# Kernel tuning notes

Measured on AMD Instinct MI355X. Metric: run time of the kernel, lower is better.

Reference implementation:

```python
import jax, jax.numpy as jnp
import numpy as np

EMBED = 256
HEADS = 8
HD = EMBED // HEADS
LEVELS = 4
POINTS = 4
FFN_H = 1024
BS = 8
LQ = 900
SHAPES = [(100, 100), (50, 50), (25, 25), (13, 13)]


def setup_inputs() -> dict:
    key = jax.random.key(0)
    ks = jax.random.split(key, 20)
    nv = sum(h * w for h, w in SHAPES)
    starts = np.cumsum([0] + [h * w for h, w in SHAPES])[:-1]
    inp = {
        "queries": jax.random.normal(ks[0], (BS, LQ, EMBED), jnp.float32),
        "memory": jax.random.normal(ks[1], (BS, nv, EMBED), jnp.float32),
        "query_pos": jax.random.normal(ks[2], (BS, LQ, EMBED), jnp.float32),
        "reference_points": jax.random.uniform(ks[3], (BS, LQ, LEVELS, 4), jnp.float32) * 0.9 + 0.05,
        "spatial_shapes": jnp.asarray(SHAPES, jnp.int32),
        "level_start_index": jnp.asarray(starts, jnp.int32),
    }
    def lin(k, din, dout):
        k1, k2 = jax.random.split(k)
        w = jax.random.normal(k1, (din, dout), jnp.float32) * 0.02
        b = jax.random.normal(k2, (dout,), jnp.float32) * 0.01
        return w, b
    specs = [("Wq", "bq", EMBED, EMBED), ("Wk", "bk", EMBED, EMBED), ("Wv", "bv", EMBED, EMBED),
             ("Wo", "bo", EMBED, EMBED), ("Wvd", "bvd", EMBED, EMBED),
             ("Woff", "boff", EMBED, HEADS * LEVELS * POINTS * 2),
             ("Watt", "batt", EMBED, HEADS * LEVELS * POINTS),
             ("Wop", "bop", EMBED, EMBED), ("Wg", "bg", 2 * EMBED, 2 * EMBED),
             ("W1", "b1", EMBED, FFN_H), ("W2", "b2", FFN_H, EMBED)]
    for i, (wn, bn, di, do) in enumerate(specs):
        w, b = lin(ks[4 + i], di, do)
        inp[wn] = w
        inp[bn] = b
    for n in ["ln1", "ln2", "ln3"]:
        inp[n + "_s"] = jnp.ones((EMBED,), jnp.float32)
        inp[n + "_b"] = jnp.zeros((EMBED,), jnp.float32)
    return inp


def _ln(x, s, b):
    m = jnp.mean(x, -1, keepdims=True)
    v = jnp.mean(jnp.square(x - m), -1, keepdims=True)
    return (x - m) * jax.lax.rsqrt(v + 1e-5) * s + b


def _bilinear(v_l, lx, ly, H, W):
    # v_l: [bs,h,H*W,hd]; lx,ly: [bs,h,lq,p] normalized in [0,1]
    # grid_sample(align_corners=False, padding=zeros) semantics
    px = lx * W - 0.5
    py = ly * H - 0.5
    x0 = jnp.floor(px)
    y0 = jnp.floor(py)
    wx = px - x0
    wy = py - y0
    x0i = x0.astype(jnp.int32)
    y0i = y0.astype(jnp.int32)
    bs, h, lq, p = lx.shape
    out = jnp.zeros((bs, h, lq, p, HD), v_l.dtype)
    for dy in (0, 1):
        for dx in (0, 1):
            xi = x0i + dx
            yi = y0i + dy
            w = (wx if dx else 1.0 - wx) * (wy if dy else 1.0 - wy)
            valid = (xi >= 0) & (xi < W) & (yi >= 0) & (yi < H)
            idx = jnp.clip(yi, 0, H - 1) * W + jnp.clip(xi, 0, W - 1)
            g = jnp.take_along_axis(v_l, idx.reshape(bs, h, lq * p)[..., None], axis=2)
            g = g.reshape(bs, h, lq, p, HD)
            out = out + w[..., None] * jnp.where(valid[..., None], g, 0.0)
    return out


def reference(queries, memory, query_pos, reference_points, spatial_shapes, level_start_index,
              Wq, bq, Wk, bk, Wv, bv, Wo, bo, Wvd, bvd, Woff, boff, Watt, batt, Wop, bop,
              Wg, bg, W1, b1, W2, b2, ln1_s, ln1_b, ln2_s, ln2_b, ln3_s, ln3_b):
    bs, lq, _ = queries.shape
    shp = np.asarray(spatial_shapes)
    st = np.asarray(level_start_index)

    # ---- self attention (pre-norm, q=k=x+pos, v=x) ----
    x = _ln(queries, ln1_s, ln1_b)
    qk = x + query_pos
    Q = (qk @ Wq + bq).reshape(bs, lq, HEADS, HD)
    K = (qk @ Wk + bk).reshape(bs, lq, HEADS, HD)
    V = (x @ Wv + bv).reshape(bs, lq, HEADS, HD)
    scores = jnp.einsum('bqhd,bkhd->bhqk', Q, K) * (1.0 / np.sqrt(HD))
    attn = jax.nn.softmax(scores, axis=-1)
    sa = jnp.einsum('bhqk,bkhd->bqhd', attn, V).reshape(bs, lq, EMBED) @ Wo + bo
    x1 = queries + sa  # dropout is identity in eval

    # ---- MS-deformable cross attention ----
    y = _ln(x1, ln2_s, ln2_b)
    qc = y + query_pos
    val = (memory @ Wvd + bvd).reshape(bs, -1, HEADS, HD).transpose(0, 2, 1, 3)  # [bs,h,Nv,hd]
    off = (qc @ Woff + boff).reshape(bs, lq, HEADS, LEVELS, POINTS, 2)
    aw = jax.nn.softmax((qc @ Watt + batt).reshape(bs, lq, HEADS, LEVELS * POINTS), axis=-1)
    aw = aw.reshape(bs, lq, HEADS, LEVELS, POINTS)
    rp = reference_points[:, :, None, :, None, :]  # [bs,lq,1,L,1,4]
    loc = rp[..., :2] + off / POINTS * rp[..., 2:] * 0.5  # [bs,lq,h,L,p,2]

    out = jnp.zeros((bs, HEADS, lq, HD), queries.dtype)
    for l in range(LEVELS):
        H, W = int(shp[l, 0]), int(shp[l, 1])
        s0 = int(st[l])
        v_l = val[:, :, s0:s0 + H * W]
        lx = jnp.transpose(loc[:, :, :, l, :, 0], (0, 2, 1, 3))  # [bs,h,lq,p]
        ly = jnp.transpose(loc[:, :, :, l, :, 1], (0, 2, 1, 3))
        samp = _bilinear(v_l, lx, ly, H, W)  # [bs,h,lq,p,hd]
        w = jnp.transpose(aw[:, :, :, l], (0, 2, 1, 3))  # [bs,h,lq,p]
        out = out + jnp.sum(w[..., None] * samp, axis=3)
    cross = out.transpose(0, 2, 1, 3).reshape(bs, lq, EMBED) @ Wop + bop

    # ---- gated fusion ----
    gi = jnp.concatenate([x1, cross], axis=-1)
    g = jax.nn.sigmoid(gi @ Wg + bg)
    x2 = g[..., :EMBED] * x1 + g[..., EMBED:] * cross

    # ---- FFN ----
    z = _ln(x2, ln3_s, ln3_b)
    ffn = jax.nn.relu(z @ W1 + b1) @ W2 + b2
    return (x2 + ffn, aw, loc)
```

## Files before the change

kernel.cpp:

```cpp
#include <hip/hip_runtime.h>
#include <hip/hip_bf16.h>
#include <math.h>

#define BB 8
#define LQ 900
#define EE 256
#define NH 8
#define HD 32
#define NL 4
#define NP 4
#define FFN_H 1024

typedef __bf16 bf16x8 __attribute__((ext_vector_type(8)));
typedef float f32x4 __attribute__((ext_vector_type(4)));
typedef unsigned short u16x8 __attribute__((ext_vector_type(8)));

__device__ __forceinline__ unsigned short f2b(float f) {
    union { float f; unsigned int u; } v; v.f = f;
    unsigned int u = v.u;
    unsigned int r = (u + 0x7fffu + ((u >> 16) & 1u)) >> 16;
    return (unsigned short)r;
}
__device__ __forceinline__ float b2f(unsigned short h) {
    union { unsigned int u; float f; } v; v.u = ((unsigned int)h) << 16; return v.f;
}

typedef __attribute__((address_space(3))) unsigned int* lds_ptr_t;
typedef const __attribute__((address_space(1))) unsigned int* gbl_ptr_t;
#define GLOAD16(g, l) __builtin_amdgcn_global_load_lds((gbl_ptr_t)(g), (lds_ptr_t)(l), 16, 0, 0)
#define VMCNT(n) asm volatile("s_waitcnt vmcnt(" #n ")" ::: "memory")

struct TDesc { const float* src; unsigned short* dst; int K, N, tile0; };
struct TPack {
    TDesc d[11];
    const float *bq, *bk, *boff, *batt;
    float *bqk, *boa;
};

__global__ __launch_bounds__(256) void prep_kernel(
    TPack p,
    const float* __restrict__ queries, const float* __restrict__ qpos,
    const float* __restrict__ ln1_s, const float* __restrict__ ln1_b,
    unsigned short* __restrict__ x_b, unsigned short* __restrict__ qk_b,
    const float* __restrict__ mem, unsigned short* __restrict__ mem_b, long memN)
{
    const int bi = blockIdx.x;
    const int t = threadIdx.x;

    if (bi < 1248) {
        int di = 0;
#pragma unroll
        for (int i = 1; i < 11; ++i) if (bi >= p.d[i].tile0) di = i;
        TDesc d = p.d[di];
        int tt = bi - d.tile0;
        int tn = (d.N + 31) >> 5;
        int tk = tt / tn, tc = tt % tn;
        __shared__ float tile[32][33];
        int tx = t & 31, ty = t >> 5;
#pragma unroll
        for (int i = 0; i < 4; ++i) {
            int kk = tk * 32 + ty + i * 8, nn = tc * 32 + tx;
            tile[ty + i * 8][tx] = d.src[(size_t)kk * d.N + nn];
        }
        __syncthreads();
#pragma unroll
        for (int i = 0; i < 4; ++i) {
            int nn = tc * 32 + ty + i * 8, kk = tk * 32 + tx;
            d.dst[(size_t)nn * d.K + kk] = f2b(tile[tx][ty + i * 8]);
        }
        return;
    }
    if (bi < 1252) {
        int which = bi - 1248;
        if (which == 0)      p.bqk[t] = p.bq[t];
        else if (which == 1) p.bqk[256 + t] = p.bk[t];
        else if (which == 2) p.boa[t] = p.boff[t];
        else if (t < 128)    p.boa[256 + t] = p.batt[t];
        return;
    }
    if (bi < 1252 + BB * LQ) {
        const int row = bi - 1252;
        const int w = t >> 6, lane = t & 63;
        __shared__ float red[4];
        float v = queries[(size_t)row * EE + t];
        float sum = v;
#pragma unroll
        for (int o = 32; o; o >>= 1) sum += __shfl_xor(sum, o, 64);
        if (lane == 0) red[w] = sum;
        __syncthreads();
        float mean = (red[0] + red[1] + red[2] + red[3]) * (1.0f / 256.0f);
        __syncthreads();
        float dd = v - mean;
        float sq = dd * dd;
#pragma unroll
        for (int o = 32; o; o >>= 1) sq += __shfl_xor(sq, o, 64);
        if (lane == 0) red[w] = sq;
        __syncthreads();
        float var = (red[0] + red[1] + red[2] + red[3]) * (1.0f / 256.0f);
        float y = dd * rsqrtf(var + 1e-5f) * ln1_s[t] + ln1_b[t];
        x_b[(size_t)row * EE + t]  = f2b(y);
        qk_b[(size_t)row * EE + t] = f2b(y + qpos[(size_t)row * EE + t]);
        return;
    }
    {
        long i = ((long)(bi - 1252 - BB * LQ) * 256 + t) * 8;
        long stride = (long)2048 * 256 * 8;
        for (; i < memN; i += stride) {
            float4 a = *(const float4*)(mem + i);
            float4 b = *(const float4*)(mem + i + 4);
            u16x8 o;
            o[0] = f2b(a.x); o[1] = f2b(a.y); o[2] = f2b(a.z); o[3] = f2b(a.w);
            o[4] = f2b(b.x); o[5] = f2b(b.y); o[6] = f2b(b.z); o[7] = f2b(b.w);
            *(u16x8*)(mem_b + i) = o;
        }
    }
}

struct GD {
    const unsigned short* A;
    const unsigned short* Bt;
    const float* bias;
    const float* resid;
    float* outF;
    unsigned short* outB;
    const float* lnS; const float* lnB; const float* lnAdd;
    unsigned short* lnOut;
    int M, K, N, ntN, tile0, ldOutB, outBoff, act;
};
struct GB { GD d[3]; int nd, tot; };

template<int BN>
__global__ __launch_bounds__(256, (BN == 128) ? 4 : 2) void gemm_pipe(GB g) {
    __shared__ __align__(16) unsigned short ldsb[2][(64 + BN) * 32];
    __shared__ float lnred[2][64][2];
    const int tid = threadIdx.x;
    const int l = tid & 63, w = tid >> 6;
    const int wr = w >> 1, wc = w & 1;
    constexpr int NJ = BN / 32;

    int t = blockIdx.x;
    if (t >= g.tot) return;
    int d = 0;
    while (d + 1 < g.nd && t >= g.d[d + 1].tile0) ++d;

    auto stage = [&](int dd, int tt, int ks, int pp) {
        const GD& D = g.d[dd];
        int local = tt - D.tile0;
        int m0 = (local / D.ntN) * 64;
        int n0 = (local % D.ntN) * BN;
        unsigned short* base = &ldsb[pp][0];
        {
            int row = w * 16 + (l >> 2);
            int rg = m0 + row; int mm = D.M - 1; rg = rg < mm ? rg : mm;
            int schunk = ((l & 3) ^ ((row >> 1) & 3)) << 4;
            GLOAD16((const char*)(D.A + (size_t)rg * D.K + (ks << 5)) + schunk,
                    base + (w * 16) * 32);
        }
#pragma unroll
        for (int ib = 0; ib < BN / 64; ++ib) {
            int row = ib * 64 + w * 16 + (l >> 2);
            int rg = n0 + row; int nn = D.N - 1; rg = rg < nn ? rg : nn;
            int schunk = ((l & 3) ^ ((row >> 1) & 3)) << 4;
            GLOAD16((const char*)(D.Bt + (size_t)rg * D.K + (ks << 5)) + schunk,
                    base + 2048 + (ib * 64 + w * 16) * 32);
        }
    };

    stage(d, t, 0, 0);
    int p = 0;

    while (true) {
        const GD D = g.d[d];
        int local = t - D.tile0;
        const int m0 = (local / D.ntN) * 64;
        const int n0 = (local % D.ntN) * BN;
        const int nk = D.K >> 5;

        f32x4 acc[2][NJ];
#pragma unroll
        for (int i = 0; i < 2; ++i)
#pragma unroll
            for (int j = 0; j < NJ; ++j) acc[i][j] = (f32x4){0.f, 0.f, 0.f, 0.f};

        for (int ks = 0; ks < nk; ++ks) {
            int nt = t, nks = ks + 1, ndd = d;
            bool have = true;
            if (nks == nk) {
                nt = t + gridDim.x; nks = 0;
                if (nt >= g.tot) have = false;
                else { while (ndd + 1 < g.nd && nt >= g.d[ndd + 1].tile0) ++ndd; }
            }
            if (have) {
                stage(ndd, nt, nks, p ^ 1);
                if constexpr (BN == 128) { VMCNT(3); } else { VMCNT(5); }
            } else {
                VMCNT(0);
            }
            __builtin_amdgcn_sched_barrier(0);
            __builtin_amdgcn_s_barrier();
            __builtin_amdgcn_sched_barrier(0);
            {
                const char* base = (const char*)&ldsb[p][0];
                const int rch = ((l >> 4) ^ ((l >> 1) & 3)) << 4;
                bf16x8 af[2];
#pragma unroll
                for (int i = 0; i < 2; ++i) {
                    int row = wr * 32 + i * 16 + (l & 15);
                    af[i] = *(const bf16x8*)(base + row * 64 + rch);
                }
#pragma unroll
                for (int j = 0; j < NJ; ++j) {
                    int row = wc * (BN / 2) + j * 16 + (l & 15);
                    bf16x8 bfr = *(const bf16x8*)(base + 4096 + row * 64 + rch);
#pragma unroll
                    for (int i = 0; i < 2; ++i)
                        acc[i][j] = __builtin_amdgcn_mfma_f32_16x16x32_bf16(af[i], bfr, acc[i][j], 0, 0, 0);
                }
            }
            __builtin_amdgcn_sched_barrier(0);
            __builtin_amdgcn_s_barrier();
            __builtin_amdgcn_sched_barrier(0);
            p ^= 1;
        }

#pragma unroll
        for (int i = 0; i < 2; ++i) {
#pragma unroll
            for (int r = 0; r < 4; ++r) {
                int gm = m0 + wr * 32 + i * 16 + ((l >> 4) << 2) + r;
                if (gm >= D.M) continue;
#pragma unroll
                for (int j = 0; j < NJ; ++j) {
                    int gn = n0 + wc * (BN / 2) + j * 16 + (l & 15);
                    if (gn >= D.N) continue;
                    float v = acc[i][j][r];
                    if (D.bias)  v += D.bias[gn];
                    if (D.resid) v += D.resid[(size_t)gm * D.N + gn];
                    if (D.act == 1)      v = fmaxf(v, 0.f);
                    else if (D.act == 2) v = 1.0f / (1.0f + __expf(-v));
                    acc[i][j][r] = v;
                    if (D.outF) D.outF[(size_t)gm * D.N + gn] = v;
                    if (D.outB) D.outB[(size_t)gm * D.ldOutB + D.outBoff + gn] = f2b(v);
                }
            }
        }

        if constexpr (BN == 256) {
            if (D.lnOut) {
#pragma unroll
                for (int i = 0; i < 2; ++i) {
#pragma unroll
                    for (int r = 0; r < 4; ++r) {
                        float s1 = 0.f, s2 = 0.f;
#pragma unroll
                        for (int j = 0; j < NJ; ++j) {
                            float v = acc[i][j][r];
                            s1 += v; s2 += v * v;
                        }
#pragma unroll
                        for (int o = 1; o <= 8; o <<= 1) {
                            s1 += __shfl_xor(s1, o, 64);
                            s2 += __shfl_xor(s2, o, 64);
                        }
                        if ((l & 15) == 0) {
                            int row = wr * 32 + i * 16 + ((l >> 4) << 2) + r;
                            lnred[wc][row][0] = s1;
                            lnred[wc][row][1] = s2;
                        }
                    }
                }
                __syncthreads();
#pragma unroll
                for (int i = 0; i < 2; ++i) {
#pragma unroll
                    for (int r = 0; r < 4; ++r) {
                        int row = wr * 32 + i * 16 + ((l >> 4) << 2) + r;
                        int gm = m0 + row;
                        if (gm >= D.M) continue;
                        float mean = (lnred[0][row][0] + lnred[1][row][0]) * (1.0f / 256.0f);
                        float msq  = (lnred[0][row][1] + lnred[1][row][1]) * (1.0f / 256.0f);
                        float rs = rsqrtf(msq - mean * mean + 1e-5f);
#pragma unroll
                        for (int j = 0; j < NJ; ++j) {
                            int gn = wc * (BN / 2) + j * 16 + (l & 15);
                            float y = (acc[i][j][r] - mean) * rs * D.lnS[gn] + D.lnB[gn]
                                      + D.lnAdd[(size_t)gm * 256 + gn];
                            D.lnOut[(size_t)gm * 256 + gn] = f2b(y);
                        }
                    }
                }
            }
        }

        t += gridDim.x;
        if (t >= g.tot) break;
        while (d + 1 < g.nd && t >= g.d[d + 1].tile0) ++d;
    }
}

__global__ __launch_bounds__(256) void attn_mfma(
    const unsigned short* __restrict__ QK, const unsigned short* __restrict__ Vb,
    unsigned short* __restrict__ outB)
{
    const int qt = blockIdx.x;
    const int bh = blockIdx.y;
    const int b = bh >> 3, h = bh & 7;
    const int tid = threadIdx.x;
    const int w = tid >> 6, l = tid & 63;

    __shared__ __align__(16) unsigned short Ks[64 * 32];
    __shared__ __align__(16) unsigned short VT[32 * 64];
    __shared__ __align__(16) unsigned short Ps[4][64 * 20];

    const int qrow_w = qt * 64 + w * 16;
    int qr = qrow_w + (l & 15); qr = qr < LQ ? qr : LQ - 1;
    bf16x8 qf = *(const bf16x8*)(QK + ((size_t)(b * LQ + qr)) * 512 + h * 32 + (l >> 4) * 8);

    f32x4 acc0 = {0.f, 0.f, 0.f, 0.f}, acc1 = {0.f, 0.f, 0.f, 0.f};
    float m_run = -1e30f, l_run = 0.f;
    const float scale = 0.17677669529663689f;
    const f32x4 z4 = {0.f, 0.f, 0.f, 0.f};

    const int key = tid >> 2;
    const int dg = (tid & 3) * 8;
    u16x8 kvc, vvc, kvn, vvn;
    {
        int krow = key; krow = krow < LQ ? krow : LQ - 1;
        size_t base = (size_t)(b * LQ + krow);
        kvc = *(const u16x8*)(QK + base * 512 + 256 + h * 32 + dg);
        vvc = *(const u16x8*)(Vb + base * 256 + h * 32 + dg);
    }

    for (int kt = 0; kt < 15; ++kt) {
        __syncthreads();
        *(u16x8*)((char*)Ks + key * 64 + ((dg * 2) ^ ((key & 3) << 4))) = kvc;
#pragma unroll
        for (int e = 0; e < 8; ++e) {
            int dd = dg + e;
            *(unsigned short*)((char*)VT + dd * 128 + ((key * 2) ^ ((dd & 7) << 4))) = vvc[e];
        }
        if (kt < 14) {
            int krow = (kt + 1) * 64 + key; krow = krow < LQ ? krow : LQ - 1;
            size_t base = (size_t)(b * LQ + krow);
            kvn = *(const u16x8*)(QK + base * 512 + 256 + h * 32 + dg);
            vvn = *(const u16x8*)(Vb + base * 256 + h * 32 + dg);
        }
        __syncthreads();

        float p[4][4];
        float tmax = -1e30f;
#pragma unroll
        for (int m = 0; m < 4; ++m) {
            int kr = m * 16 + (l & 15);
            bf16x8 kf = *(const bf16x8*)((const char*)Ks + kr * 64 +
                        (((l >> 4) * 16) ^ ((kr & 3) << 4)));
            f32x4 sf = __builtin_amdgcn_mfma_f32_16x16x32_bf16(kf, qf, z4, 0, 0, 0);
#pragma unroll
            for (int r = 0; r < 4; ++r) {
                int kk = kt * 64 + m * 16 + (l >> 4) * 4 + r;
                float sv = (kk < LQ) ? sf[r] * scale : -1e30f;
                p[m][r] = sv;
                tmax = fmaxf(tmax, sv);
            }
        }
        tmax = fmaxf(tmax, __shfl_xor(tmax, 16, 64));
        tmax = fmaxf(tmax, __shfl_xor(tmax, 32, 64));
        float newm = fmaxf(m_run, tmax);
        float corr = __expf(m_run - newm);
        m_run = newm;
        float tsum = 0.f;
#pragma unroll
        for (int m = 0; m < 4; ++m)
#pragma unroll
            for (int r = 0; r < 4; ++r) {
                float e = __expf(p[m][r] - newm);
                p[m][r] = e;
                tsum += e;
            }
        tsum += __shfl_xor(tsum, 16, 64);
        tsum += __shfl_xor(tsum, 32, 64);
        l_run = l_run * corr + tsum;
        acc0 *= corr;
        acc1 *= corr;

        unsigned short* pw = &Ps[w][0];
#pragma unroll
        for (int m = 0; m < 4; ++m)
#pragma unroll
            for (int r = 0; r < 4; ++r) {
                int kk = m * 16 + (l >> 4) * 4 + r;
                pw[kk * 20 + (l & 15)] = f2b(p[m][r]);
            }

#pragma unroll
        for (int s = 0; s < 2; ++s) {
            union { unsigned short u[8]; bf16x8 v; } pb;
#pragma unroll
            for (int j = 0; j < 8; ++j)
                pb.u[j] = pw[(s * 32 + (l >> 4) * 8 + j) * 20 + (l & 15)];
#pragma unroll
            for (int m2 = 0; m2 < 2; ++m2) {
                int dd = m2 * 16 + (l & 15);
                bf16x8 vf = *(const bf16x8*)((const char*)VT + dd * 128 +
                            ((s * 64 + (l >> 4) * 16) ^ ((dd & 7) << 4)));
                if (m2 == 0) acc0 = __builtin_amdgcn_mfma_f32_16x16x32_bf16(vf, pb.v, acc0, 0, 0, 0);
                else         acc1 = __builtin_amdgcn_mfma_f32_16x16x32_bf16(vf, pb.v, acc1, 0, 0, 0);
            }
        }
        if (kt < 14) { kvc = kvn; vvc = vvn; }
    }

    float inv = 1.0f / l_run;
    int q = qrow_w + (l & 15);
    if (q < LQ) {
        size_t obase = ((size_t)(b * LQ + q)) * 256 + h * 32;
#pragma unroll
        for (int r = 0; r < 4; ++r) {
            int d0 = (l >> 4) * 4 + r;
            outB[obase + d0]      = f2b(acc0[r] * inv);
            outB[obase + 16 + d0] = f2b(acc1[r] * inv);
        }
    }
}

__global__ __launch_bounds__(256) void sample_fused(
    const float* __restrict__ off_att, const float* __restrict__ refp,
    const unsigned short* __restrict__ val,
    const int* __restrict__ shapes, const int* __restrict__ starts,
    float* __restrict__ aw_out, float* __restrict__ loc_out,
    unsigned short* __restrict__ samp, int NV)
{
    const int row = blockIdx.x;
    const int b = row / LQ;
    const int t = threadIdx.x;
    const int h = t >> 5, d = t & 31;

    __shared__ float l_logit[128];
    __shared__ float l_aw[128];
    __shared__ float l_loc[256];
    __shared__ int l_sh[NL * 2];
    __shared__ int l_st[NL];

    if (t < 128) l_logit[t] = off_att[(size_t)row * 384 + 256 + t];
    {
        float o = off_att[(size_t)row * 384 + t];
        int c = t & 1;
        int lv = (t >> 3) & 3;
        float rc = refp[((size_t)row * 4 + lv) * 4 + c];
        float rs = refp[((size_t)row * 4 + lv) * 4 + 2 + c];
        float loc = rc + o * 0.125f * rs;
        l_loc[t] = loc;
        loc_out[(size_t)row * 256 + t] = loc;
    }
    if (t < NL * 2) l_sh[t] = shapes[t];
    if (t < NL) l_st[t] = starts[t];
    __syncthreads();
    if (t < 128) {
        int hh = t >> 4;
        float mx = -1e30f;
#pragma unroll
        for (int i = 0; i < 16; ++i) mx = fmaxf(mx, l_logit[hh * 16 + i]);
        float sum = 0.f;
#pragma unroll
        for (int i = 0; i < 16; ++i) sum += __expf(l_logit[hh * 16 + i] - mx);
        float aw = __expf(l_logit[t] - mx) / sum;
        l_aw[t] = aw;
        aw_out[(size_t)row * 128 + t] = aw;
    }
    __syncthreads();

    float acc = 0.f;
    const unsigned short* vb = val + (size_t)b * NV * EE + h * HD + d;

#pragma unroll
    for (int lv = 0; lv < NL; ++lv) {
        const int Hh = l_sh[lv * 2], Ww = l_sh[lv * 2 + 1];
        const int s0 = l_st[lv];
#pragma unroll
        for (int p = 0; p < NP; ++p) {
            const int base = ((h * NL + lv) * NP + p) * 2;
            float lx = l_loc[base], ly = l_loc[base + 1];
            float wgt0 = l_aw[h * 16 + lv * NP + p];
            float px = lx * (float)Ww - 0.5f;
            float py = ly * (float)Hh - 0.5f;
            float x0f = floorf(px), y0f = floorf(py);
            float wx = px - x0f, wy = py - y0f;
            int x0 = (int)x0f, y0 = (int)y0f;
#pragma unroll
            for (int dy = 0; dy < 2; ++dy) {
                int yi = y0 + dy;
                bool vy = (yi >= 0) && (yi < Hh);
                int yc = min(max(yi, 0), Hh - 1);
                float wyv = dy ? wy : 1.f - wy;
#pragma unroll
                for (int dx = 0; dx < 2; ++dx) {
                    int xi = x0 + dx;
                    bool vv = vy && (xi >= 0) && (xi < Ww);
                    int xc = min(max(xi, 0), Ww - 1);
                    float wgt = wgt0 * wyv * (dx ? wx : 1.f - wx);
                    float gv = b2f(vb[(size_t)(s0 + yc * Ww + xc) * EE]);
                    acc += vv ? wgt * gv : 0.f;
                }
            }
        }
    }
    samp[(size_t)row * EE + t] = f2b(acc);
}

__global__ __launch_bounds__(256) void gate_ln3(
    const float* __restrict__ g, const float* __restrict__ x1,
    const float* __restrict__ cross, const float* __restrict__ s,
    const float* __restrict__ bln, float* __restrict__ x2out,
    unsigned short* __restrict__ zb)
{
    const int row = blockIdx.x;
    const int t = threadIdx.x;
    const int w = t >> 6;
    const int lane = t & 63;
    __shared__ float red[4];

    float g1 = g[(size_t)row * 512 + t];
    float g2 = g[(size_t)row * 512 + 256 + t];
    float v = g1 * x1[(size_t)row * EE + t] + g2 * cross[(size_t)row * EE + t];
    x2out[(size_t)row * EE + t] = v;

    float sum = v;
#pragma unroll
    for (int o = 32; o; o >>= 1) sum += __shfl_xor(sum, o, 64);
    if (lane == 0) red[w] = sum;
    __syncthreads();
    float mean = (red[0] + red[1] + red[2] + red[3]) * (1.0f / 256.0f);
    __syncthreads();

    float d = v - mean;
    float sq = d * d;
#pragma unroll
    for (int o = 32; o; o >>= 1) sq += __shfl_xor(sq, o, 64);
    if (lane == 0) red[w] = sq;
    __syncthreads();
    float var = (red[0] + red[1] + red[2] + red[3]) * (1.0f / 256.0f);

    float y = d * rsqrtf(var + 1e-5f) * s[t] + bln[t];
    zb[(size_t)row * EE + t] = f2b(y);
}

extern "C" void kernel_launch(void* const* d_in, const int* in_sizes, int n_in,
                              void* d_out, int out_size, void* d_ws, size_t ws_size,
                              hipStream_t stream)
{
    const float* queries   = (const float*)d_in[0];
    const float* memory    = (const float*)d_in[1];
    const float* query_pos = (const float*)d_in[2];
    const float* refp      = (const float*)d_in[3];
    const int*   shapes    = (const int*)d_in[4];
    const int*   starts    = (const int*)d_in[5];
    const float* Wq  = (const float*)d_in[6],  *bq  = (const float*)d_in[7];
    const float* Wk  = (const float*)d_in[8],  *bk  = (const float*)d_in[9];
    const float* Wv  = (const float*)d_in[10], *bv  = (const float*)d_in[11];
    const float* Wo  = (const float*)d_in[12], *bo  = (const float*)d_in[13];
    const float* Wvd = (const float*)d_in[14], *bvd = (const float*)d_in[15];
    const float* Woff= (const float*)d_in[16], *boff= (const float*)d_in[17];
    const float* Watt= (const float*)d_in[18], *batt= (const float*)d_in[19];
    const float* Wop = (const float*)d_in[20], *bop = (const float*)d_in[21];
    const float* Wg  = (const float*)d_in[22], *bg  = (const float*)d_in[23];
    const float* W1  = (const float*)d_in[24], *b1  = (const float*)d_in[25];
    const float* W2  = (const float*)d_in[26], *b2  = (const float*)d_in[27];
    const float* ln1_s = (const float*)d_in[28], *ln1_b = (const float*)d_in[29];
    const float* ln2_s = (const float*)d_in[30], *ln2_b = (const float*)d_in[31];
    const float* ln3_s = (const float*)d_in[32], *ln3_b = (const float*)d_in[33];

    const int NV = in_sizes[1] / (BB * EE);
    const int Mq = BB * LQ;
    const int Mv = BB * NV;
    const long memN = (long)Mv * EE;

    char* W8 = (char*)d_ws;
    size_t off = 0;
    auto alloc = [&](size_t bytes) { char* p = W8 + off; off += (bytes + 255) & ~(size_t)255; return p; };

    unsigned short* mem_b = (unsigned short*)alloc((size_t)memN * 2);
    unsigned short* val_b = (unsigned short*)alloc((size_t)memN * 2);
    unsigned short* WtQK  = (unsigned short*)alloc(512 * 256 * 2);
    unsigned short* WtV   = (unsigned short*)alloc(256 * 256 * 2);
    unsigned short* WtO   = (unsigned short*)alloc(256 * 256 * 2);
    unsigned short* WtVD  = (unsigned short*)alloc(256 * 256 * 2);
    unsigned short* WtOA  = (unsigned short*)alloc(384 * 256 * 2);
    unsigned short* WtOP  = (unsigned short*)alloc(256 * 256 * 2);
    unsigned short* WtG   = (unsigned short*)alloc(512 * 512 * 2);
    unsigned short* Wt1   = (unsigned short*)alloc(1024 * 256 * 2);
    unsigned short* Wt2   = (unsigned short*)alloc(256 * 1024 * 2);
    float*          bqk   = (float*)alloc(512 * 4);
    float*          boa   = (float*)alloc(384 * 4);
    unsigned short* qkb   = (unsigned short*)alloc((size_t)Mq * 512 * 2);
    unsigned short* vb_buf= (unsigned short*)alloc((size_t)Mq * 256 * 2);
    unsigned short* av_buf= (unsigned short*)alloc((size_t)Mq * 256 * 2);
    float*          x1    = (float*)alloc((size_t)Mq * 256 * 4);
    unsigned short* xc_cat= (unsigned short*)alloc((size_t)Mq * 512 * 2);
    unsigned short* qc_b  = (unsigned short*)alloc((size_t)Mq * 256 * 2);
    unsigned short* qk_b  = (unsigned short*)alloc((size_t)Mq * 256 * 2);
    float*          cross = (float*)alloc((size_t)Mq * 256 * 4);

    unsigned short* x_b = (unsigned short*)cross;
    float* off_att = (float*)qkb;
    unsigned short* samp_b = av_buf;
    float* gbuf = (float*)mem_b;
    float* x2   = (float*)((char*)mem_b + (size_t)Mq * 512 * 4);
    unsigned short* z_b = (unsigned short*)((char*)x2 + (size_t)Mq * 256 * 4);
    unsigned short* hidden_b = (unsigned short*)((char*)z_b + (size_t)Mq * 256 * 2);

    float* out0    = (float*)d_out;
    float* aw_out  = out0 + (size_t)Mq * 256;
    float* loc_out = aw_out + (size_t)Mq * 128;

    dim3 blk(256);
    const int tMq = (Mq + 63) / 64;
    const int tv  = (Mv + 63) / 64;

    TPack tp;
    tp.d[0]  = { Wq,   WtQK,             256, 256,    0 };
    tp.d[1]  = { Wk,   WtQK + 256 * 256, 256, 256,   64 };
    tp.d[2]  = { Wv,   WtV,              256, 256,  128 };
    tp.d[3]  = { Wo,   WtO,              256, 256,  192 };
    tp.d[4]  = { Wvd,  WtVD,             256, 256,  256 };
    tp.d[5]  = { Woff, WtOA,             256, 256,  320 };
    tp.d[6]  = { Watt, WtOA + 256 * 256, 256, 128,  384 };
    tp.d[7]  = { Wop,  WtOP,             256, 256,  416 };
    tp.d[8]  = { Wg,   WtG,              512, 512,  480 };
    tp.d[9]  = { W1,   Wt1,              256, 1024, 736 };
    tp.d[10] = { W2,   Wt2,             1024, 256,  992 };
    tp.bq = bq; tp.bk = bk; tp.boff = boff; tp.batt = batt;
    tp.bqk = bqk; tp.boa = boa;
    prep_kernel<<<1252 + Mq + 2048, blk, 0, stream>>>(
        tp, queries, query_pos, ln1_s, ln1_b, x_b, qk_b, memory, mem_b, memN);

    {
        GB g; g.nd = 3;
        g.d[0] = { mem_b, WtVD, bvd, nullptr, nullptr, val_b,
                   nullptr, nullptr, nullptr, nullptr,
                   Mv, 256, 256, 2, 0, 256, 0, 0 };
        g.d[1] = { qk_b, WtQK, bqk, nullptr, nullptr, qkb,
                   nullptr, nullptr, nullptr, nullptr,
                   Mq, 256, 512, 4, tv * 2, 512, 0, 0 };
        g.d[2] = { x_b, WtV, bv, nullptr, nullptr, vb_buf,
                   nullptr, nullptr, nullptr, nullptr,
                   Mq, 256, 256, 2, tv * 2 + tMq * 4, 256, 0, 0 };
        g.tot = tv * 2 + tMq * 6;
        gemm_pipe<128><<<1536, blk, 0, stream>>>(g);
    }

    attn_mfma<<<dim3(15, BB * NH), blk, 0, stream>>>(qkb, vb_buf, av_buf);

    {
        GB g; g.nd = 1;
        g.d[0] = { av_buf, WtO, bo, queries, x1, xc_cat,
                   ln2_s, ln2_b, query_pos, qc_b,
                   Mq, 256, 256, 1, 0, 512, 0, 0 };
        g.tot = tMq;
        gemm_pipe<256><<<tMq, blk, 0, stream>>>(g);
    }

    {
        GB g; g.nd = 1;
        g.d[0] = { qc_b, WtOA, boa, nullptr, off_att, nullptr,
                   nullptr, nullptr, nullptr, nullptr,
                   Mq, 256, 384, 3, 0, 384, 0, 0 };
        g.tot = tMq * 3;
        gemm_pipe<128><<<tMq * 3, blk, 0, stream>>>(g);
    }

    sample_fused<<<Mq, blk, 0, stream>>>(off_att, refp, val_b, shapes, starts,
                                         aw_out, loc_out, samp_b, NV);

    {
        GB g; g.nd = 1;
        g.d[0] = { samp_b, WtOP, bop, nullptr, cross, xc_cat,
                   nullptr, nullptr, nullptr, nullptr,
                   Mq, 256, 256, 2, 0, 512, 256, 0 };
        g.tot = tMq * 2;
        gemm_pipe<128><<<tMq * 2, blk, 0, stream>>>(g);
    }

    {
        GB g; g.nd = 1;
        g.d[0] = { xc_cat, WtG, bg, nullptr, gbuf, nullptr,
                   nullptr, nullptr, nullptr, nullptr,
                   Mq, 512, 512, 4, 0, 512, 0, 2 };
        g.tot = tMq * 4;
        gemm_pipe<128><<<tMq * 4, blk, 0, stream>>>(g);
    }

    gate_ln3<<<Mq, blk, 0, stream>>>(gbuf, x1, cross, ln3_s, ln3_b, x2, z_b);

    {
        GB g; g.nd = 1;
        g.d[0] = { z_b, Wt1, b1, nullptr, nullptr, hidden_b,
                   nullptr, nullptr, nullptr, nullptr,
                   Mq, 256, 1024, 8, 0, 1024, 0, 1 };
        g.tot = tMq * 8;
        gemm_pipe<128><<<tMq * 8, blk, 0, stream>>>(g);
    }

    {
        GB g; g.nd = 1;
        g.d[0] = { hidden_b, Wt2, b2, x2, out0, nullptr,
                   nullptr, nullptr, nullptr, nullptr,
                   Mq, 1024, 256, 2, 0, 256, 0, 0 };
        g.tot = tMq * 2;
        gemm_pipe<128><<<tMq * 2, blk, 0, stream>>>(g);
    }
}
```

Measured before the change: 333.6 us.

## Fuse fp32-to-bf16 memory conversion into value-projection GEMM A-tile loads

Removes the separate pass in the prep kernel that converted the whole fp32 memory tensor to bf16. The value GEMM now reads fp32 rows directly into registers, converts them and writes the swizzled bf16 A tile into LDS after the MFMA step. The value projection is split into its own launch with BN=256, apart from the QK/V projections. This saves a full write and re-read of a bf16 copy of memory, at the cost of more register pressure, extra LDS stores and lgkm waits inside the GEMM loop, and an extra kernel launch.

```diff
diff --git a/kernel.cpp b/kernel.cpp
--- a/kernel.cpp
+++ b/kernel.cpp
@@ -29,6 +29,7 @@
 typedef const __attribute__((address_space(1))) unsigned int* gbl_ptr_t;
 #define GLOAD16(g, l) __builtin_amdgcn_global_load_lds((gbl_ptr_t)(g), (lds_ptr_t)(l), 16, 0, 0)
 #define VMCNT(n) asm volatile("s_waitcnt vmcnt(" #n ")" ::: "memory")
+#define LGKM0()  asm volatile("s_waitcnt lgkmcnt(0)" ::: "memory")
 
 struct TDesc { const float* src; unsigned short* dst; int K, N, tile0; };
 struct TPack {
@@ -41,8 +42,7 @@
     TPack p,
     const float* __restrict__ queries, const float* __restrict__ qpos,
     const float* __restrict__ ln1_s, const float* __restrict__ ln1_b,
-    unsigned short* __restrict__ x_b, unsigned short* __restrict__ qk_b,
-    const float* __restrict__ mem, unsigned short* __restrict__ mem_b, long memN)
+    unsigned short* __restrict__ x_b, unsigned short* __restrict__ qk_b)
 {
     const int bi = blockIdx.x;
     const int t = threadIdx.x;
@@ -78,7 +78,7 @@
         else if (t < 128)    p.boa[256 + t] = p.batt[t];
         return;
     }
-    if (bi < 1252 + BB * LQ) {
+    {
         const int row = bi - 1252;
         const int w = t >> 6, lane = t & 63;
         __shared__ float red[4];
@@ -100,24 +100,12 @@
         float y = dd * rsqrtf(var + 1e-5f) * ln1_s[t] + ln1_b[t];
         x_b[(size_t)row * EE + t]  = f2b(y);
         qk_b[(size_t)row * EE + t] = f2b(y + qpos[(size_t)row * EE + t]);
-        return;
-    }
-    {
-        long i = ((long)(bi - 1252 - BB * LQ) * 256 + t) * 8;
-        long stride = (long)2048 * 256 * 8;
-        for (; i < memN; i += stride) {
-            float4 a = *(const float4*)(mem + i);
-            float4 b = *(const float4*)(mem + i + 4);
-            u16x8 o;
-            o[0] = f2b(a.x); o[1] = f2b(a.y); o[2] = f2b(a.z); o[3] = f2b(a.w);
-            o[4] = f2b(b.x); o[5] = f2b(b.y); o[6] = f2b(b.z); o[7] = f2b(b.w);
-            *(u16x8*)(mem_b + i) = o;
-        }
     }
 }
 
 struct GD {
     const unsigned short* A;
+    const float* Af;
     const unsigned short* Bt;
     const float* bias;
     const float* resid;
@@ -129,7 +117,7 @@
 };
 struct GB { GD d[3]; int nd, tot; };
 
-template<int BN>
+template<int BN, bool AF32>
 __global__ __launch_bounds__(256, (BN == 128) ? 4 : 2) void gemm_pipe(GB g) {
     __shared__ __align__(16) unsigned short ldsb[2][(64 + BN) * 32];
     __shared__ float lnred[2][64][2];
@@ -143,13 +131,23 @@
     int d = 0;
     while (d + 1 < g.nd && t >= g.d[d + 1].tile0) ++d;
 
+    const int sc = tid & 3;
+    float4 fA[2];
+
     auto stage = [&](int dd, int tt, int ks, int pp) {
         const GD& D = g.d[dd];
         int local = tt - D.tile0;
         int m0 = (local / D.ntN) * 64;
         int n0 = (local % D.ntN) * BN;
         unsigned short* base = &ldsb[pp][0];
-        {
+        if constexpr (AF32) {
+            int row = tid >> 2;
+            int rg = m0 + row; int mm = D.M - 1; rg = rg < mm ? rg : mm;
+            int ck = (sc ^ ((row >> 1) & 3)) * 8;
+            const float* src = D.Af + (size_t)rg * D.K + (ks << 5) + ck;
+            fA[0] = *(const float4*)src;
+            fA[1] = *(const float4*)(src + 4);
+        } else {
             int row = w * 16 + (l >> 2);
             int rg = m0 + row; int mm = D.M - 1; rg = rg < mm ? rg : mm;
             int schunk = ((l & 3) ^ ((row >> 1) & 3)) << 4;
@@ -165,8 +163,16 @@
                     base + 2048 + (ib * 64 + w * 16) * 32);
         }
     };
+    auto commitA = [&](int pp) {
+        int row = tid >> 2;
+        u16x8 o;
+        o[0] = f2b(fA[0].x); o[1] = f2b(fA[0].y); o[2] = f2b(fA[0].z); o[3] = f2b(fA[0].w);
+        o[4] = f2b(fA[1].x); o[5] = f2b(fA[1].y); o[6] = f2b(fA[1].z); o[7] = f2b(fA[1].w);
+        *(u16x8*)((char*)&ldsb[pp][0] + row * 64 + sc * 16) = o;
+    };
 
     stage(d, t, 0, 0);
+    if constexpr (AF32) { commitA(0); LGKM0(); }
     int p = 0;
 
     while (true) {
@@ -192,7 +198,9 @@
             }
             if (have) {
                 stage(ndd, nt, nks, p ^ 1);
-                if constexpr (BN == 128) { VMCNT(3); } else { VMCNT(5); }
+                if constexpr (AF32)          { VMCNT(6); }
+                else if constexpr (BN == 128){ VMCNT(3); }
+                else                         { VMCNT(5); }
             } else {
                 VMCNT(0);
             }
@@ -216,6 +224,9 @@
                     for (int i = 0; i < 2; ++i)
                         acc[i][j] = __builtin_amdgcn_mfma_f32_16x16x32_bf16(af[i], bfr, acc[i][j], 0, 0, 0);
                 }
+            }
+            if constexpr (AF32) {
+                if (have) { commitA(p ^ 1); LGKM0(); }
             }
             __builtin_amdgcn_sched_barrier(0);
             __builtin_amdgcn_s_barrier();
@@ -245,7 +256,7 @@
             }
         }
 
-        if constexpr (BN == 256) {
+        if constexpr (BN == 256 && !AF32) {
             if (D.lnOut) {
 #pragma unroll
                 for (int i = 0; i < 2; ++i) {
@@ -578,7 +589,6 @@
     size_t off = 0;
     auto alloc = [&](size_t bytes) { char* p = W8 + off; off += (bytes + 255) & ~(size_t)255; return p; };
 
-    unsigned short* mem_b = (unsigned short*)alloc((size_t)memN * 2);
     unsigned short* val_b = (unsigned short*)alloc((size_t)memN * 2);
     unsigned short* WtQK  = (unsigned short*)alloc(512 * 256 * 2);
     unsigned short* WtV   = (unsigned short*)alloc(256 * 256 * 2);
@@ -603,8 +613,8 @@
     unsigned short* x_b = (unsigned short*)cross;
     float* off_att = (float*)qkb;
     unsigned short* samp_b = av_buf;
-    float* gbuf = (float*)mem_b;
-    float* x2   = (float*)((char*)mem_b + (size_t)Mq * 512 * 4);
+    float* gbuf = (float*)val_b;
+    float* x2   = (float*)((char*)val_b + (size_t)Mq * 512 * 4);
     unsigned short* z_b = (unsigned short*)((char*)x2 + (size_t)Mq * 256 * 4);
     unsigned short* hidden_b = (unsigned short*)((char*)z_b + (size_t)Mq * 256 * 2);
 
@@ -630,42 +640,48 @@
     tp.d[10] = { W2,   Wt2,             1024, 256,  992 };
     tp.bq = bq; tp.bk = bk; tp.boff = boff; tp.batt = batt;
     tp.bqk = bqk; tp.boa = boa;
-    prep_kernel<<<1252 + Mq + 2048, blk, 0, stream>>>(
-        tp, queries, query_pos, ln1_s, ln1_b, x_b, qk_b, memory, mem_b, memN);
-
-    {
-        GB g; g.nd = 3;
-        g.d[0] = { mem_b, WtVD, bvd, nullptr, nullptr, val_b,
+    prep_kernel<<<1252 + Mq, blk, 0, stream>>>(
+        tp, queries, query_pos, ln1_s, ln1_b, x_b, qk_b);
+
+    {
+        GB g; g.nd = 2;
+        g.d[0] = { qk_b, nullptr, WtQK, bqk, nullptr, nullptr, qkb,
                    nullptr, nullptr, nullptr, nullptr,
-                   Mv, 256, 256, 2, 0, 256, 0, 0 };
-        g.d[1] = { qk_b, WtQK, bqk, nullptr, nullptr, qkb,
+                   Mq, 256, 512, 4, 0, 512, 0, 0 };
+        g.d[1] = { x_b, nullptr, WtV, bv, nullptr, nullptr, vb_buf,
                    nullptr, nullptr, nullptr, nullptr,
-                   Mq, 256, 512, 4, tv * 2, 512, 0, 0 };
-        g.d[2] = { x_b, WtV, bv, nullptr, nullptr, vb_buf,
+                   Mq, 256, 256, 2, tMq * 4, 256, 0, 0 };
+        g.tot = tMq * 6;
+        gemm_pipe<128, false><<<g.tot, blk, 0, stream>>>(g);
+    }
+
+    {
+        GB g; g.nd = 1;
+        g.d[0] = { nullptr, memory, WtVD, bvd, nullptr, nullptr, val_b,
                    nullptr, nullptr, nullptr, nullptr,
-                   Mq, 256, 256, 2, tv * 2 + tMq * 4, 256, 0, 0 };
-        g.tot = tv * 2 + tMq * 6;
-        gemm_pipe<128><<<1536, blk, 0, stream>>>(g);
+                   Mv, 256, 256, 1, 0, 256, 0, 0 };
+        g.tot = tv;
+        gemm_pipe<256, true><<<831, blk, 0, stream>>>(g);
     }
 
     attn_mfma<<<dim3(15, BB * NH), blk, 0, stream>>>(qkb, vb_buf, av_buf);
 
     {
         GB g; g.nd = 1;
-        g.d[0] = { av_buf, WtO, bo, queries, x1, xc_cat,
+        g.d[0] = { av_buf, nullptr, WtO, bo, queries, x1, xc_cat,
                    ln2_s, ln2_b, query_pos, qc_b,
                    Mq, 256, 256, 1, 0, 512, 0, 0 };
         g.tot = tMq;
-        gemm_pipe<256><<<tMq, blk, 0, stream>>>(g);
+        gemm_pipe<256, false><<<tMq, blk, 0, stream>>>(g);
     }
 
     {
         GB g; g.nd = 1;
-        g.d[0] = { qc_b, WtOA, boa, nullptr, off_att, nullptr,
+        g.d[0] = { qc_b, nullptr, WtOA, boa, nullptr, off_att, nullptr,
                    nullptr, nullptr, nullptr, nullptr,
                    Mq, 256, 384, 3, 0, 384, 0, 0 };
         g.tot = tMq * 3;
-        gemm_pipe<128><<<tMq * 3, blk, 0, stream>>>(g);
+        gemm_pipe<128, false><<<g.tot, blk, 0, stream>>>(g);
     }
 
     sample_fused<<<Mq, blk, 0, stream>>>(off_att, refp, val_b, shapes, starts,
@@ -673,39 +689,39 @@
 
     {
         GB g; g.nd = 1;
-        g.d[0] = { samp_b, WtOP, bop, nullptr, cross, xc_cat,
+        g.d[0] = { samp_b, nullptr, WtOP, bop, nullptr, cross, xc_cat,
                    nullptr, nullptr, nullptr, nullptr,
                    Mq, 256, 256, 2, 0, 512, 256, 0 };
         g.tot = tMq * 2;
-        gemm_pipe<128><<<tMq * 2, blk, 0, stream>>>(g);
+        gemm_pipe<128, false><<<g.tot, blk, 0, stream>>>(g);
     }
 
     {
         GB g; g.nd = 1;
-        g.d[0] = { xc_cat, WtG, bg, nullptr, gbuf, nullptr,
+        g.d[0] = { xc_cat, nullptr, WtG, bg, nullptr, gbuf, nullptr,
                    nullptr, nullptr, nullptr, nullptr,
                    Mq, 512, 512, 4, 0, 512, 0, 2 };
         g.tot = tMq * 4;
-        gemm_pipe<128><<<tMq * 4, blk, 0, stream>>>(g);
+        gemm_pipe<128, false><<<g.tot, blk, 0, stream>>>(g);
     }
 
     gate_ln3<<<Mq, blk, 0, stream>>>(gbuf, x1, cross, ln3_s, ln3_b, x2, z_b);
 
     {
         GB g; g.nd = 1;
-        g.d[0] = { z_b, Wt1, b1, nullptr, nullptr, hidden_b,
+        g.d[0] = { z_b, nullptr, Wt1, b1, nullptr, nullptr, hidden_b,
                    nullptr, nullptr, nullptr, nullptr,
                    Mq, 256, 1024, 8, 0, 1024, 0, 1 };
         g.tot = tMq * 8;
-        gemm_pipe<128><<<tMq * 8, blk, 0, stream>>>(g);
+        gemm_pipe<128, false><<<g.tot, blk, 0, stream>>>(g);
     }
 
     {
         GB g; g.nd = 1;
-        g.d[0] = { hidden_b, Wt2, b2, x2, out0, nullptr,
+        g.d[0] = { hidden_b, nullptr, Wt2, b2, x2, out0, nullptr,
                    nullptr, nullptr, nullptr, nullptr,
                    Mq, 1024, 256, 2, 0, 256, 0, 0 };
         g.tot = tMq * 2;
-        gemm_pipe<128><<<tMq * 2, blk, 0, stream>>>(g);
+        gemm_pipe<128, false><<<g.tot, blk, 0, stream>>>(g);
     }
 }
```

After: 328.1 us. About the same (-1.7%).
